# Optimization experiments

Measured on AMD Instinct MI355X. Metric: run time of the kernel, lower is better.

Reference implementation:

```python
import jax, jax.numpy as jnp
import numpy as np

N = 100000; R2 = 500; H = 200; T = 3; E = 300000; R2E = 400000
SE = 4000; SR = 8; S2E = 8000
SLOPE = (1.0 / 8 + 1.0 / 3) / 2  # eval-mode F.rrelu negative slope


def l2norm(x):
    # F.normalize(x) along dim=1 with eps=1e-12
    return x / jnp.maximum(jnp.linalg.norm(x, axis=-1, keepdims=True), 1e-12)


def rrelu(x):
    return jnp.where(x >= 0, x, x * SLOPE)


def seg_mean(vals, seg, num):
    # mean of vals rows grouped by seg id; absent groups stay zero (matches x_input init)
    s = jax.ops.segment_sum(vals, seg, num_segments=num)
    c = jax.ops.segment_sum(jnp.ones((vals.shape[0],), vals.dtype), seg, num_segments=num)
    return s / jnp.maximum(c, 1.0)[:, None]


def lstm_cell(x, h, c, Wih, Whh, bih, bhh):
    g = x @ Wih.T + bih + h @ Whh.T + bhh
    i, f, gg, o = jnp.split(g, 4, axis=1)
    c2 = jax.nn.sigmoid(f) * c + jax.nn.sigmoid(i) * jnp.tanh(gg)
    return jax.nn.sigmoid(o) * jnp.tanh(c2), c2


def gru_cell(x, h, Wih, Whh, bih, bhh):
    gi = x @ Wih.T + bih
    gh = h @ Whh.T + bhh
    ir, iz, inn = jnp.split(gi, 3, axis=1)
    hr, hz, hn = jnp.split(gh, 3, axis=1)
    r = jax.nn.sigmoid(ir + hr)
    z = jax.nn.sigmoid(iz + hz)
    n = jnp.tanh(inn + r * hn)
    return (1 - z) * n + z * h


def rgcn_layer(h, rel_emb, src, dst, et, Wn, Wloop, Wevolve, num_nodes):
    # UnionRGCNLayer: msg = (h_src + rel_emb[etype]) @ W_neighbor, sum-aggregated at dst;
    # self loop uses evolve weight for nodes with in-edges, plain loop weight otherwise.
    msg = (h[src] + rel_emb[et]) @ Wn
    agg = jax.ops.segment_sum(msg, dst, num_segments=num_nodes)
    indeg = jax.ops.segment_sum(jnp.ones((src.shape[0],), h.dtype), dst, num_segments=num_nodes)
    loop = jnp.where((indeg > 0)[:, None], h @ Wevolve, h @ Wloop)
    return rrelu(agg + loop)


def setup_inputs() -> dict:
    key = jax.random.key(0)
    ks = iter(jax.random.split(key, 48))
    s = 1.0 / np.sqrt(H)
    d = {}
    d['src'] = jax.random.randint(next(ks), (T, E), 0, N)
    d['dst'] = jax.random.randint(next(ks), (T, E), 0, N)
    d['etype'] = jax.random.randint(next(ks), (T, E), 0, R2)
    d['r_to_e'] = jax.random.randint(next(ks), (T, R2E), 0, N)
    d['r_seg'] = jax.random.randint(next(ks), (T, R2E), 0, R2)
    d['s_src'] = jax.random.randint(next(ks), (T, SE), 0, R2)
    d['s_dst'] = jax.random.randint(next(ks), (T, SE), 0, R2)
    d['s_etype'] = jax.random.randint(next(ks), (T, SE), 0, SR)
    d['s_r_to_e'] = jax.random.randint(next(ks), (T, S2E), 0, R2)
    d['s_r_seg'] = jax.random.randint(next(ks), (T, S2E), 0, SR)
    d['dynamic_emb'] = jax.random.normal(next(ks), (N, H), jnp.float32)
    d['emb_rel'] = jax.random.normal(next(ks), (R2, H), jnp.float32) * s
    d['p_rel'] = jax.random.normal(next(ks), (SR, H), jnp.float32) * s
    d['Wih1'] = jax.random.normal(next(ks), (4 * H, 2 * H), jnp.float32) * s
    d['Whh1'] = jax.random.normal(next(ks), (4 * H, H), jnp.float32) * s
    d['bih1'] = jax.random.normal(next(ks), (4 * H,), jnp.float32) * s
    d['bhh1'] = jax.random.normal(next(ks), (4 * H,), jnp.float32) * s
    d['Wih2'] = jax.random.normal(next(ks), (4 * H, 2 * H), jnp.float32) * s
    d['Whh2'] = jax.random.normal(next(ks), (4 * H, H), jnp.float32) * s
    d['bih2'] = jax.random.normal(next(ks), (4 * H,), jnp.float32) * s
    d['bhh2'] = jax.random.normal(next(ks), (4 * H,), jnp.float32) * s
    d['Wih3'] = jax.random.normal(next(ks), (3 * H, H), jnp.float32) * s
    d['Whh3'] = jax.random.normal(next(ks), (3 * H, H), jnp.float32) * s
    d['bih3'] = jax.random.normal(next(ks), (3 * H,), jnp.float32) * s
    d['bhh3'] = jax.random.normal(next(ks), (3 * H,), jnp.float32) * s
    d['Wihe'] = jax.random.normal(next(ks), (3 * H, H), jnp.float32) * s
    d['Whhe'] = jax.random.normal(next(ks), (3 * H, H), jnp.float32) * s
    d['bihe'] = jax.random.normal(next(ks), (3 * H,), jnp.float32) * s
    d['bhhe'] = jax.random.normal(next(ks), (3 * H,), jnp.float32) * s
    for nm in ('Wn', 'Wl', 'We', 'sWn', 'sWl', 'sWe'):
        d[nm] = jax.random.normal(next(ks), (2, H, H), jnp.float32) * s
    return d


def reference(src, dst, etype, r_to_e, r_seg, s_src, s_dst, s_etype, s_r_to_e, s_r_seg,
              dynamic_emb, emb_rel, p_rel,
              Wih1, Whh1, bih1, bhh1, Wih2, Whh2, bih2, bhh2,
              Wih3, Whh3, bih3, bhh3, Wihe, Whhe, bihe, bhhe,
              Wn, Wl, We, sWn, sWl, sWe):
    h = l2norm(dynamic_emb)  # layer_norm=True path
    h_0 = c_0 = p_h_0 = p_c_0 = None
    history_embs = []
    rel_embs = []
    for t in range(T):
        # per-relation mean of involved entity embeddings (r_to_e grouped by uniq_r)
        x_input = seg_mean(h[r_to_e[t]], r_seg[t], R2)
        if t == 0:
            h_prev, c_prev = emb_rel, x_input
        else:
            h_prev, c_prev = h_0, c_0
        x_cat = jnp.concatenate([emb_rel, x_input], axis=1)
        h_0, c_0 = lstm_cell(x_cat, h_prev, c_prev, Wih1, Whh1, bih1, bhh1)
        h_0 = l2norm(h_0); c_0 = l2norm(c_0)
        # super-graph: per-super-relation mean of relation embeddings
        sx = seg_mean(h_0[s_r_to_e[t]], s_r_seg[t], SR)
        if t == 0:
            ph_prev, pc_prev = p_rel, sx
        else:
            ph_prev, pc_prev = p_h_0, p_c_0
        sx_cat = jnp.concatenate([p_rel, sx], axis=1)
        p_h_0, p_c_0 = lstm_cell(sx_cat, ph_prev, pc_prev, Wih2, Whh2, bih2, bhh2)
        p_h_0 = l2norm(p_h_0); p_c_0 = l2norm(p_c_0)
        # super RGCN over relation-nodes (2 UnionRGCN layers, same rel emb per layer)
        cur = h_0
        for l in range(2):
            cur = rgcn_layer(cur, p_h_0, s_src[t], s_dst[t], s_etype[t], sWn[l], sWl[l], sWe[l], R2)
        cur = l2norm(cur)
        h_0 = gru_cell(cur, h_0, Wih3, Whh3, bih3, bhh3)
        h_0 = l2norm(h_0)
        rel_embs.append(h_0)
        # entity RGCN over the snapshot graph
        cur_h = h
        for l in range(2):
            cur_h = rgcn_layer(cur_h, h_0, src[t], dst[t], etype[t], Wn[l], Wl[l], We[l], N)
        cur_h = l2norm(cur_h)
        h = gru_cell(cur_h, h, Wihe, Whhe, bihe, bhhe)
        h = l2norm(h)
        history_embs.append(h)
    return jnp.stack(history_embs), jnp.stack(rel_embs)
```

## Files before the change

kernel.cpp:

```cpp
#include <hip/hip_runtime.h>
#include <math.h>

#define N_NODES 100000
#define H 200
#define R2 500
#define T_STEPS 3
#define E_EDGES 300000
#define R2E 400000
#define SE_EDGES 4000
#define SR 8
#define S2E 8000
#define SLOPE 0.22916666666666666f
#define NB 64
#define RCHUNK ((R2E + NB - 1) / NB)
#define NCH 128
#define CHSZ ((N_NODES + NCH - 1) / NCH)
#define SPT  ((CHSZ + 255) / 256)

typedef unsigned short u16;
typedef unsigned int u32;
typedef __bf16 bf8 __attribute__((ext_vector_type(8)));
typedef float f32x4 __attribute__((ext_vector_type(4)));

static __device__ __forceinline__ float fsig(float x) { return 1.f / (1.f + __expf(-x)); }
static __device__ __forceinline__ float ftanh(float x) {
    float e = __expf(-2.f * fabsf(x));
    float t = (1.f - e) / (1.f + e);
    return (x >= 0.f) ? t : -t;
}
static __device__ __forceinline__ float bf2f(u32 lo16) {
    u32 v = lo16 << 16; float f; __builtin_memcpy(&f, &v, 4); return f;
}
static __device__ __forceinline__ u16 f2bf(float a) {
    __bf16 x = (__bf16)a; u16 u; __builtin_memcpy(&u, &x, 2); return u;
}
static __device__ __forceinline__ u32 pk2(float a, float b) {
    return (u32)f2bf(a) | ((u32)f2bf(b) << 16);
}
static __device__ __forceinline__ int xcd_swz(int b, int nwg) {
    int q = nwg >> 3, r = nwg & 7;
    int xcd = b & 7, u = b >> 3;
    int start = xcd * q + (xcd < r ? xcd : r);
    return start + u;
}

__global__ __launch_bounds__(256) void l2norm_k(const float* __restrict__ src, float* __restrict__ dst,
                                                u16* __restrict__ mir, int rows) {
    int wave = threadIdx.x >> 6, lane = threadIdx.x & 63;
    int r = blockIdx.x * 4 + wave;
    if (r >= rows) return;
    float4 v = make_float4(0.f, 0.f, 0.f, 0.f);
    if (lane < 50) v = *(const float4*)(src + (size_t)r * H + lane * 4);
    float s = v.x * v.x + v.y * v.y + v.z * v.z + v.w * v.w;
    for (int o = 32; o > 0; o >>= 1) s += __shfl_down(s, o);
    float rn = 1.f / fmaxf(sqrtf(__shfl(s, 0)), 1e-12f);
    if (lane < 50) {
        float4 o4 = make_float4(v.x * rn, v.y * rn, v.z * rn, v.w * rn);
        *(float4*)(dst + (size_t)r * H + lane * 4) = o4;
        if (mir) {
            uint2 u; u.x = pk2(o4.x, o4.y); u.y = pk2(o4.z, o4.w);
            *(uint2*)(mir + (size_t)r * H + lane * 4) = u;
        }
    }
}

__global__ __launch_bounds__(256) void l2norm_b_k(u16* __restrict__ buf, int rows) {
    int wave = threadIdx.x >> 6, lane = threadIdx.x & 63;
    int r = blockIdx.x * 4 + wave;
    if (r >= rows) return;
    uint2 u = make_uint2(0, 0);
    if (lane < 50) u = *(const uint2*)(buf + (size_t)r * H + lane * 4);
    float x0 = bf2f(u.x & 0xffff), x1 = bf2f(u.x >> 16);
    float x2 = bf2f(u.y & 0xffff), x3 = bf2f(u.y >> 16);
    float s = x0 * x0 + x1 * x1 + x2 * x2 + x3 * x3;
    for (int o = 32; o > 0; o >>= 1) s += __shfl_down(s, o);
    float rn = 1.f / fmaxf(sqrtf(__shfl(s, 0)), 1e-12f);
    if (lane < 50) {
        uint2 o2; o2.x = pk2(x0 * rn, x1 * rn); o2.y = pk2(x2 * rn, x3 * rn);
        *(uint2*)(buf + (size_t)r * H + lane * 4) = o2;
    }
}

__global__ __launch_bounds__(256) void l2norm_bb_k(const u16* __restrict__ src, float* __restrict__ dst,
                                                   u16* __restrict__ mir, int rows) {
    int wave = threadIdx.x >> 6, lane = threadIdx.x & 63;
    int r = blockIdx.x * 4 + wave;
    if (r >= rows) return;
    uint2 u = make_uint2(0, 0);
    if (lane < 50) u = *(const uint2*)(src + (size_t)r * H + lane * 4);
    float x0 = bf2f(u.x & 0xffff), x1 = bf2f(u.x >> 16);
    float x2 = bf2f(u.y & 0xffff), x3 = bf2f(u.y >> 16);
    float s = x0 * x0 + x1 * x1 + x2 * x2 + x3 * x3;
    for (int o = 32; o > 0; o >>= 1) s += __shfl_down(s, o);
    float rn = 1.f / fmaxf(sqrtf(__shfl(s, 0)), 1e-12f);
    if (lane < 50) {
        float4 o4 = make_float4(x0 * rn, x1 * rn, x2 * rn, x3 * rn);
        *(float4*)(dst + (size_t)r * H + lane * 4) = o4;
        uint2 o2; o2.x = pk2(o4.x, o4.y); o2.y = pk2(o4.z, o4.w);
        *(uint2*)(mir + (size_t)r * H + lane * 4) = o2;
    }
}

__global__ void wconv4_k(const float* __restrict__ W0, const float* __restrict__ W1,
                         const float* __restrict__ W2, const float* __restrict__ W3,
                         u16* __restrict__ o) {
    int m = blockIdx.y;
    const float* W = (m == 0) ? W0 : (m == 1) ? W1 : (m == 2) ? W2 : W3;
    int i = blockIdx.x * 256 + threadIdx.x;
    if (i < 40000) { int n = i / 200, k = i - n * 200; o[m * 40000 + i] = f2bf(W[k * 200 + n]); }
}
__global__ void wconv2_k(const float* __restrict__ Wa, const float* __restrict__ Wb, u16* __restrict__ o) {
    int i = blockIdx.x * 256 + threadIdx.x;
    if (i < 240000) o[i] = f2bf(i < 120000 ? Wa[i] : Wb[i - 120000]);
}

__global__ void cnt3_k(const int* __restrict__ d, int total, int per_t, int stride, int* __restrict__ cnt) {
    int i = blockIdx.x * 256 + threadIdx.x;
    if (i < total) { int t = i / per_t; atomicAdd(&cnt[t * stride + d[i]], 1); }
}

__global__ __launch_bounds__(256) void seg_cnt3_k(const int* __restrict__ seg, int per_t, int nseg,
                                                  int blocks_per_t, int* __restrict__ cnt) {
    __shared__ int lc[500];
    int t = blockIdx.x / blocks_per_t;
    int pb = blockIdx.x - t * blocks_per_t;
    const int* s = seg + (size_t)t * per_t;
    int* c = cnt + (size_t)t * nseg;
    for (int i = threadIdx.x; i < nseg; i += 256) lc[i] = 0;
    __syncthreads();
    int chunk = (per_t + blocks_per_t - 1) / blocks_per_t;
    int beg = pb * chunk;
    int end = beg + chunk; if (end > per_t) end = per_t;
    for (int i = beg + threadIdx.x; i < end; i += 256) atomicAdd(&lc[s[i]], 1);
    __syncthreads();
    for (int i = threadIdx.x; i < nseg; i += 256) if (lc[i]) atomicAdd(&c[i], lc[i]);
}

__global__ __launch_bounds__(256) void hist3_k(const int* __restrict__ seg,
                                               int* __restrict__ hist, int* __restrict__ cnt) {
    __shared__ int lc[R2];
    int t = blockIdx.x / NB;
    int pb = blockIdx.x - t * NB;
    const int* s = seg + (size_t)t * R2E;
    for (int i = threadIdx.x; i < R2; i += 256) lc[i] = 0;
    __syncthreads();
    int beg = pb * RCHUNK;
    int end = beg + RCHUNK; if (end > R2E) end = R2E;
    for (int i = beg + threadIdx.x; i < end; i += 256) atomicAdd(&lc[s[i]], 1);
    __syncthreads();
    int* hrow = hist + (size_t)(t * NB + pb) * R2;
    int* c = cnt + (size_t)t * R2;
    for (int i = threadIdx.x; i < R2; i += 256) {
        hrow[i] = lc[i];
        if (lc[i]) atomicAdd(&c[i], lc[i]);
    }
}

__global__ __launch_bounds__(1024) void scan3_k(const int* __restrict__ cntA, int* __restrict__ offA,
                                                int* __restrict__ curA, int n) {
    const int b = blockIdx.x;
    const int* cnt = cntA + (size_t)b * n;
    int* off = offA + (size_t)b * (n + 1);
    int* cur = curA + (size_t)b * n;
    __shared__ int part[1024];
    int tid = threadIdx.x;
    int per = (n + 1023) / 1024;
    int s0 = tid * per;
    int e0 = s0 + per; if (e0 > n) e0 = n;
    int sum = 0;
    for (int i = s0; i < e0; ++i) sum += cnt[i];
    part[tid] = sum;
    __syncthreads();
    for (int d = 1; d < 1024; d <<= 1) {
        int v = (tid >= d) ? part[tid - d] : 0;
        __syncthreads();
        part[tid] += v;
        __syncthreads();
    }
    int excl = (tid == 0) ? 0 : part[tid - 1];
    for (int i = s0; i < e0; ++i) { off[i] = excl; cur[i] = excl; excl += cnt[i]; }
    if (tid == 1023) off[n] = excl;
}

__global__ __launch_bounds__(256) void scanA_k(const int* __restrict__ cntA, int* __restrict__ bsum, int n) {
    int b = blockIdx.x;
    int t = b / NCH, ch = b - t * NCH;
    const int* cnt = cntA + (size_t)t * n;
    int base = ch * CHSZ;
    int cend = base + CHSZ; if (cend > n) cend = n;
    int s0 = base + threadIdx.x * SPT;
    int e0 = s0 + SPT; if (e0 > cend) e0 = cend;
    int sum = 0;
    for (int i = s0; i < e0 && i < cend; ++i) sum += cnt[i];
    __shared__ int red[256];
    red[threadIdx.x] = (s0 < cend) ? sum : 0;
    __syncthreads();
    for (int o = 128; o > 0; o >>= 1) {
        if (threadIdx.x < o) red[threadIdx.x] += red[threadIdx.x + o];
        __syncthreads();
    }
    if (threadIdx.x == 0) bsum[t * NCH + ch] = red[0];
}

__global__ __launch_bounds__(128) void scanB_k(const int* __restrict__ bsum, int* __restrict__ boff,
                                               int* __restrict__ offA, int n) {
    int t = blockIdx.x;
    int tid = threadIdx.x;
    __shared__ int part[128];
    int v = bsum[t * NCH + tid];
    part[tid] = v;
    __syncthreads();
    for (int d = 1; d < 128; d <<= 1) {
        int u = (tid >= d) ? part[tid - d] : 0;
        __syncthreads();
        part[tid] += u;
        __syncthreads();
    }
    boff[t * NCH + tid] = part[tid] - v;
    if (tid == 127) offA[(size_t)t * (n + 1) + n] = part[127];
}

__global__ __launch_bounds__(256) void scanC_k(const int* __restrict__ cntA, const int* __restrict__ boff,
                                               int* __restrict__ offA, int* __restrict__ curA, int n) {
    int b = blockIdx.x;
    int t = b / NCH, ch = b - t * NCH;
    const int* cnt = cntA + (size_t)t * n;
    int* off = offA + (size_t)t * (n + 1);
    int* cur = curA + (size_t)t * n;
    int base = ch * CHSZ;
    int cend = base + CHSZ; if (cend > n) cend = n;
    int s0 = base + threadIdx.x * SPT;
    int e0 = s0 + SPT; if (e0 > cend) e0 = cend;
    int sum = 0;
    for (int i = s0; i < e0 && i < cend; ++i) sum += cnt[i];
    __shared__ int part[256];
    int my = (s0 < cend) ? sum : 0;
    part[threadIdx.x] = my;
    __syncthreads();
    for (int d = 1; d < 256; d <<= 1) {
        int u = (threadIdx.x >= d) ? part[threadIdx.x - d] : 0;
        __syncthreads();
        part[threadIdx.x] += u;
        __syncthreads();
    }
    int excl = boff[t * NCH + ch] + part[threadIdx.x] - my;
    for (int i = s0; i < e0 && i < cend; ++i) {
        off[i] = excl; cur[i] = excl; excl += cnt[i];
    }
}

__global__ __launch_bounds__(64) void offs3_k(const int* __restrict__ hist, const int* __restrict__ csr,
                                              int* __restrict__ offb) {
    int b = blockIdx.x;
    int t = b / R2, s = b - t * R2;
    int lane = threadIdx.x;
    int v = hist[(size_t)(t * NB + lane) * R2 + s];
    int pre = v;
    for (int o = 1; o < 64; o <<= 1) {
        int u = __shfl_up(pre, o);
        if (lane >= o) pre += u;
    }
    int base = csr[(size_t)t * (R2 + 1) + s];
    offb[(size_t)(t * NB + lane) * R2 + s] = base + pre - v;
}

__global__ __launch_bounds__(256) void part3_k(const int* __restrict__ seg, const int* __restrict__ val,
                                               const int* __restrict__ offb, int* __restrict__ outp) {
    __shared__ int cur[R2];
    int t = blockIdx.x / NB;
    int pb = blockIdx.x - t * NB;
    const int* s = seg + (size_t)t * R2E;
    const int* v = val + (size_t)t * R2E;
    const int* ob = offb + (size_t)(t * NB + pb) * R2;
    int* o = outp + (size_t)t * R2E;
    for (int i = threadIdx.x; i < R2; i += 256) cur[i] = ob[i];
    __syncthreads();
    int beg = pb * RCHUNK;
    int end = beg + RCHUNK; if (end > R2E) end = R2E;
    for (int i = beg + threadIdx.x; i < end; i += 256) {
        int p = atomicAdd(&cur[s[i]], 1);
        o[p] = v[i];
    }
}

__global__ void scatter3_k(const int* __restrict__ dst, const int* __restrict__ src,
                           const int* __restrict__ et, int* __restrict__ cur,
                           int* __restrict__ psrc, int* __restrict__ pet,
                           int per_t, int stride, int total) {
    int i = blockIdx.x * 256 + threadIdx.x;
    if (i < total) {
        int t = i / per_t;
        int p = atomicAdd(&cur[t * stride + dst[i]], 1);
        psrc[(size_t)t * per_t + p] = src[i];
        pet[(size_t)t * per_t + p] = et[i];
    }
}

__global__ __launch_bounds__(256) void zlist3b_k(const int* __restrict__ cnt, int* __restrict__ zl,
                                                 int* __restrict__ nz, int n, int bpt) {
    int t = blockIdx.x / bpt;
    int pb = blockIdx.x - t * bpt;
    int i = pb * 256 + threadIdx.x;
    bool z = (i < n) && (cnt[(size_t)t * n + i] == 0);
    unsigned long long mask = __ballot(z);
    int wave = threadIdx.x >> 6, lane = threadIdx.x & 63;
    __shared__ int wbase[4];
    __shared__ int bbase;
    if (lane == 0) wbase[wave] = __popcll(mask);
    __syncthreads();
    if (threadIdx.x == 0) {
        int s0 = wbase[0], s1 = wbase[1], s2 = wbase[2], s3 = wbase[3];
        int tot = s0 + s1 + s2 + s3;
        bbase = tot ? atomicAdd(&nz[t], tot) : 0;
        wbase[0] = 0; wbase[1] = s0; wbase[2] = s0 + s1; wbase[3] = s0 + s1 + s2;
    }
    __syncthreads();
    if (z) {
        int off = bbase + wbase[wave] + __popcll(mask & ((1ull << lane) - 1ull));
        zl[(size_t)t * n + off] = i;
    }
}

#define SEG_CW 25
__global__ __launch_bounds__(256) void seg_acc_k(const float* __restrict__ hsrc,
                                                 const int* __restrict__ idx,
                                                 const int* __restrict__ seg, int n,
                                                 float* __restrict__ acc, int nseg) {
    __shared__ float lacc[500 * SEG_CW];
    int cg = blockIdx.x & 7;
    int pb = blockIdx.x >> 3;
    int NPB = gridDim.x >> 3;
    int t = threadIdx.x;
    for (int i = t; i < nseg * SEG_CW; i += 256) lacc[i] = 0.f;
    __syncthreads();
    int chunk = (n + NPB - 1) / NPB;
    int beg = pb * chunk;
    int end = beg + chunk; if (end > n) end = n;
    if (t < 250) {
        int il = t / SEG_CW;
        int c = t - il * SEG_CW;
        int col = cg * SEG_CW + c;
        for (int i = beg + il; i < end; i += 10) {
            int r = seg[i];
            int e = idx[i];
            atomicAdd(&lacc[r * SEG_CW + c], hsrc[(size_t)e * H + col]);
        }
    }
    __syncthreads();
    for (int i = t; i < nseg * SEG_CW; i += 256) {
        int r = i / SEG_CW, c = i - (i / SEG_CW) * SEG_CW;
        atomicAdd(&acc[(size_t)r * H + cg * SEG_CW + c], lacc[i]);
    }
}

__global__ void seg_div_k(float* __restrict__ acc, const int* __restrict__ cnt, int rows) {
    int i = blockIdx.x * blockDim.x + threadIdx.x;
    if (i < rows * H) {
        int c = cnt[i / H];
        acc[i] /= (float)(c > 0 ? c : 1);
    }
}

__global__ __launch_bounds__(256) void seg_mean_part_k(const u16* __restrict__ h,
                                                       const int* __restrict__ per,
                                                       const int* __restrict__ off,
                                                       float* __restrict__ xacc, int nseg) {
    int r = blockIdx.x >> 2;
    int p = blockIdx.x & 3;
    if (r >= nseg) return;
    int wv = threadIdx.x >> 6, lane = threadIdx.x & 63;
    int beg = off[r], end = off[r + 1];
    float a0 = 0.f, a1 = 0.f, a2 = 0.f, a3 = 0.f;
    for (int i = beg + p * 4 + wv; i < end; i += 16) {
        int e = per[i];
        if (lane < 50) {
            uint2 u = ((const uint2*)(h + (size_t)e * H))[lane];
            a0 += bf2f(u.x & 0xffff); a1 += bf2f(u.x >> 16);
            a2 += bf2f(u.y & 0xffff); a3 += bf2f(u.y >> 16);
        }
    }
    __shared__ float red[4][200];
    if (lane < 50) *(float4*)(&red[wv][lane * 4]) = make_float4(a0, a1, a2, a3);
    __syncthreads();
    int t = threadIdx.x;
    if (t < 200) {
        float s = red[0][t] + red[1][t] + red[2][t] + red[3][t];
        atomicAdd(&xacc[(size_t)r * H + t], s);
    }
}
__global__ void seg_fin_k(float* __restrict__ acc, const int* __restrict__ off, int nseg) {
    int i = blockIdx.x * 256 + threadIdx.x;
    if (i < nseg * H) {
        int r = i / H;
        int c = off[r + 1] - off[r];
        acc[i] /= (float)(c > 0 ? c : 1);
    }
}

__global__ __launch_bounds__(256) void lstm_k(const float* __restrict__ x1, const float* __restrict__ x2,
                                              const float* __restrict__ hprev, const float* __restrict__ cprev,
                                              const float* __restrict__ Wih, const float* __restrict__ Whh,
                                              const float* __restrict__ bih, const float* __restrict__ bhh,
                                              float* __restrict__ hout, float* __restrict__ cout, int rows) {
    int r = blockIdx.x;
    if (r >= rows) return;
    __shared__ float xb[2 * H], hb[H], gb[4 * H], hv[H], cv[H];
    __shared__ float red[8];
    int t = threadIdx.x;
    for (int i = t; i < 2 * H; i += 256)
        xb[i] = (i < H) ? x1[(size_t)r * H + i] : x2[(size_t)r * H + i - H];
    if (t < H) hb[t] = hprev[(size_t)r * H + t];
    __syncthreads();
    for (int j = t; j < 4 * H; j += 256) {
        float s = bih[j] + bhh[j];
        const float* wi = Wih + (size_t)j * 2 * H;
        for (int k = 0; k < 2 * H; ++k) s += xb[k] * wi[k];
        const float* wh = Whh + (size_t)j * H;
        for (int k = 0; k < H; ++k) s += hb[k] * wh[k];
        gb[j] = s;
    }
    __syncthreads();
    if (t < H) {
        float ig = fsig(gb[t]);
        float fg = fsig(gb[H + t]);
        float gg = ftanh(gb[2 * H + t]);
        float og = fsig(gb[3 * H + t]);
        float c2 = fg * cprev[(size_t)r * H + t] + ig * gg;
        cv[t] = c2;
        hv[t] = og * ftanh(c2);
    }
    __syncthreads();
    float sh = 0.f, sc = 0.f;
    if (t < H) { sh = hv[t] * hv[t]; sc = cv[t] * cv[t]; }
    for (int o = 32; o > 0; o >>= 1) { sh += __shfl_down(sh, o); sc += __shfl_down(sc, o); }
    if ((t & 63) == 0) { red[t >> 6] = sh; red[4 + (t >> 6)] = sc; }
    __syncthreads();
    if (t == 0) {
        red[0] = 1.f / fmaxf(sqrtf(red[0] + red[1] + red[2] + red[3]), 1e-12f);
        red[4] = 1.f / fmaxf(sqrtf(red[4] + red[5] + red[6] + red[7]), 1e-12f);
    }
    __syncthreads();
    if (t < H) {
        hout[(size_t)r * H + t] = hv[t] * red[0];
        cout[(size_t)r * H + t] = cv[t] * red[4];
    }
}

__global__ __launch_bounds__(256) void gru_small_k(const float* __restrict__ x, const float* __restrict__ h,
                                                   const float* __restrict__ Wih, const float* __restrict__ Whh,
                                                   const float* __restrict__ bih, const float* __restrict__ bhh,
                                                   float* __restrict__ outp, u16* __restrict__ mirp, int rows) {
    int r = blockIdx.x;
    if (r >= rows) return;
    __shared__ float xb[H], hb[H], gi[3 * H], gh[3 * H], ov[H];
    __shared__ float red[4];
    int t = threadIdx.x;
    if (t < H) { xb[t] = x[(size_t)r * H + t]; hb[t] = h[(size_t)r * H + t]; }
    __syncthreads();
    for (int j = t; j < 3 * H; j += 256) {
        float si = bih[j], sh2 = bhh[j];
        const float* wi = Wih + (size_t)j * H;
        const float* wh = Whh + (size_t)j * H;
        for (int k = 0; k < H; ++k) { si += xb[k] * wi[k]; sh2 += hb[k] * wh[k]; }
        gi[j] = si; gh[j] = sh2;
    }
    __syncthreads();
    if (t < H) {
        float rr = fsig(gi[t] + gh[t]);
        float zz = fsig(gi[H + t] + gh[H + t]);
        float nn = ftanh(gi[2 * H + t] + rr * gh[2 * H + t]);
        ov[t] = (1.f - zz) * nn + zz * hb[t];
    }
    __syncthreads();
    float s = (t < H) ? ov[t] * ov[t] : 0.f;
    for (int o = 32; o > 0; o >>= 1) s += __shfl_down(s, o);
    if ((t & 63) == 0) red[t >> 6] = s;
    __syncthreads();
    if (t == 0) red[0] = 1.f / fmaxf(sqrtf(red[0] + red[1] + red[2] + red[3]), 1e-12f);
    __syncthreads();
    if (t < H) {
        float v = ov[t] * red[0];
        outp[(size_t)r * H + t] = v;
        mirp[(size_t)r * H + t] = f2bf(v);
    }
}

__global__ __launch_bounds__(256) void sup_agg_csr_k(const float* __restrict__ cur, const float* __restrict__ prel,
                                                     const int* __restrict__ soff, const int* __restrict__ sssrc,
                                                     const int* __restrict__ sset, float* __restrict__ sagg) {
    int r = blockIdx.x;
    int t = threadIdx.x;
    if (t >= H) return;
    int beg = soff[r], end = soff[r + 1];
    float acc = 0.f;
    for (int i = beg; i < end; ++i) {
        int s = sssrc[i], et = sset[i];
        acc += cur[(size_t)s * H + t] + prel[(size_t)et * H + t];
    }
    sagg[(size_t)r * H + t] = acc;
}

__global__ __launch_bounds__(256) void sup_comb_k(const float* __restrict__ agg, const float* __restrict__ cur,
                                                  const float* __restrict__ Wn, const float* __restrict__ We,
                                                  const float* __restrict__ Wl, const int* __restrict__ indeg,
                                                  float* __restrict__ outp) {
    int r = blockIdx.x;
    __shared__ float ar[H], cr[H];
    int t = threadIdx.x;
    if (t < H) { ar[t] = agg[(size_t)r * H + t]; cr[t] = cur[(size_t)r * H + t]; }
    __syncthreads();
    const float* W2 = (indeg[r] > 0) ? We : Wl;
    if (t < H) {
        float s = 0.f;
        for (int k = 0; k < H; ++k) s += ar[k] * Wn[(size_t)k * H + t] + cr[k] * W2[(size_t)k * H + t];
        outp[(size_t)r * H + t] = (s >= 0.f) ? s : s * SLOPE;
    }
}

__global__ __launch_bounds__(256) void ent_agg_b_k(const u16* __restrict__ cur, const u16* __restrict__ rel,
                                                   const int* __restrict__ eoff, const int* __restrict__ esrc,
                                                   const int* __restrict__ eet, u16* __restrict__ agg, int n) {
    int wave = threadIdx.x >> 6, lane = threadIdx.x & 63;
    int v = blockIdx.x * 4 + wave;
    if (v >= n) return;
    float a0 = 0.f, a1 = 0.f, a2 = 0.f, a3 = 0.f;
    bool act = lane < 50;
    int beg = eoff[v], end = eoff[v + 1];
    int i = beg;
    for (; i + 2 <= end; i += 2) {
        int e0 = esrc[i], t0 = eet[i];
        int e1 = esrc[i + 1], t1 = eet[i + 1];
        if (act) {
            uint2 h0 = ((const uint2*)(cur + (size_t)e0 * H))[lane];
            uint2 h1 = ((const uint2*)(cur + (size_t)e1 * H))[lane];
            uint2 r0 = ((const uint2*)(rel + (size_t)t0 * H))[lane];
            uint2 r1 = ((const uint2*)(rel + (size_t)t1 * H))[lane];
            a0 += bf2f(h0.x & 0xffff) + bf2f(r0.x & 0xffff) + bf2f(h1.x & 0xffff) + bf2f(r1.x & 0xffff);
            a1 += bf2f(h0.x >> 16) + bf2f(r0.x >> 16) + bf2f(h1.x >> 16) + bf2f(r1.x >> 16);
            a2 += bf2f(h0.y & 0xffff) + bf2f(r0.y & 0xffff) + bf2f(h1.y & 0xffff) + bf2f(r1.y & 0xffff);
            a3 += bf2f(h0.y >> 16) + bf2f(r0.y >> 16) + bf2f(h1.y >> 16) + bf2f(r1.y >> 16);
        }
    }
    if (i < end) {
        int e0 = esrc[i], t0 = eet[i];
        if (act) {
            uint2 h0 = ((const uint2*)(cur + (size_t)e0 * H))[lane];
            uint2 r0 = ((const uint2*)(rel + (size_t)t0 * H))[lane];
            a0 += bf2f(h0.x & 0xffff) + bf2f(r0.x & 0xffff);
            a1 += bf2f(h0.x >> 16) + bf2f(r0.x >> 16);
            a2 += bf2f(h0.y & 0xffff) + bf2f(r0.y & 0xffff);
            a3 += bf2f(h0.y >> 16) + bf2f(r0.y >> 16);
        }
    }
    if (act) {
        uint2 o; o.x = pk2(a0, a1); o.y = pk2(a2, a3);
        ((uint2*)(agg + (size_t)v * H))[lane] = o;
    }
}

#define BSTR 108
__global__ __launch_bounds__(128) void gemm_bp_k(const u16* __restrict__ A1, const u16* __restrict__ A2,
                                                 const u16* __restrict__ B1, const u16* __restrict__ B2,
                                                 u16* __restrict__ Cm, int M, int Nc) {
    __shared__ __bf16 Bs[64 * BSTR];
    const int tid = threadIdx.x;
    int idx2 = xcd_swz(blockIdx.x, gridDim.x);
    const int m0 = (idx2 >> 2) * 128;
    const int n0 = (idx2 & 3) * 64;
    const int w = tid >> 6, lane = tid & 63;
    const int lr = lane & 15, lo = lane >> 4;
    const int mbase = m0 + w * 64;

    bf8 zb;
#pragma unroll
    for (int e = 0; e < 8; ++e) zb[e] = (__bf16)0.f;

    f32x4 acc[4][4];
#pragma unroll
    for (int i = 0; i < 4; ++i)
#pragma unroll
        for (int j = 0; j < 4; ++j)
#pragma unroll
            for (int e = 0; e < 4; ++e) acc[i][j][e] = 0.f;

    auto stageB = [&](const u16* Bp, int kbase, int nch) {
        for (int ch = tid; ch < 64 * nch; ch += 128) {
            int n = ch / nch, q = ch - n * nch;
            int ng = n0 + n;
            uint4 v = make_uint4(0, 0, 0, 0);
            if (ng < Nc) v = *(const uint4*)(Bp + (size_t)ng * 200 + kbase + q * 8);
            *(uint4*)(&Bs[n * BSTR + q * 8]) = v;
        }
    };
    auto loadA = [&](bf8* buf, const u16* Ap, int kt7) {
        int kk = kt7 * 32 + lo * 8;
        bool kv = kk < 200;
#pragma unroll
        for (int mf = 0; mf < 4; ++mf) {
            int m = mbase + mf * 16 + lr;
            bf8 v = zb;
            if (kv && m < M) v = *(const bf8*)(Ap + (size_t)m * 200 + kk);
            buf[mf] = v;
        }
    };
    auto mmaStep = [&](bf8* a, int kt7, int kbase) {
        int kk = kt7 * 32 + lo * 8;
        int kcl = (kk < 200) ? (kk - kbase) : 0;
#pragma unroll
        for (int nf = 0; nf < 4; ++nf) {
            bf8 b = *(const bf8*)(&Bs[(nf * 16 + lr) * BSTR + kcl]);
#pragma unroll
            for (int mf = 0; mf < 4; ++mf)
                acc[mf][nf] = __builtin_amdgcn_mfma_f32_16x16x32_bf16(a[mf], b, acc[mf][nf], 0, 0, 0);
        }
    };

    bf8 a0[4], a1[4];
    stageB(B1, 0, 12);
    __syncthreads();
    loadA(a0, A1, 0);
    loadA(a1, A1, 1); mmaStep(a0, 0, 0);
    loadA(a0, A1, 2); mmaStep(a1, 1, 0);
    loadA(a1, A1, 3); mmaStep(a0, 2, 0);
    __syncthreads();
    stageB(B1, 96, 13);
    __syncthreads();
    loadA(a0, A1, 4); mmaStep(a1, 3, 96);
    loadA(a1, A1, 5); mmaStep(a0, 4, 96);
    loadA(a0, A1, 6); mmaStep(a1, 5, 96);
    loadA(a1, A2, 0); mmaStep(a0, 6, 96);
    __syncthreads();
    stageB(B2, 0, 12);
    __syncthreads();
    loadA(a0, A2, 1); mmaStep(a1, 0, 0);
    loadA(a1, A2, 2); mmaStep(a0, 1, 0);
    loadA(a0, A2, 3); mmaStep(a1, 2, 0);
    __syncthreads();
    stageB(B2, 96, 13);
    __syncthreads();
    loadA(a1, A2, 4); mmaStep(a0, 3, 96);
    loadA(a0, A2, 5); mmaStep(a1, 4, 96);
    loadA(a1, A2, 6); mmaStep(a0, 5, 96);
    mmaStep(a1, 6, 96);

#pragma unroll
    for (int mf = 0; mf < 4; ++mf) {
#pragma unroll
        for (int r = 0; r < 4; ++r) {
            int m = mbase + mf * 16 + lo * 4 + r;
            if (m >= M) continue;
#pragma unroll
            for (int nf = 0; nf < 4; ++nf) {
                int n = n0 + nf * 16 + lr;
                if (n >= Nc) continue;
                float v = acc[mf][nf][r];
                v = (v >= 0.f) ? v : v * SLOPE;
                Cm[(size_t)m * Nc + n] = f2bf(v);
            }
        }
    }
}

__global__ __launch_bounds__(256) void fixup_b_k(const u16* __restrict__ h, const float* __restrict__ Wl,
                                                 const int* __restrict__ zl, const int* __restrict__ nz,
                                                 u16* __restrict__ outp) {
    __shared__ float xr[H];
    int nzv = *nz;
    for (int z = blockIdx.x; z < nzv; z += gridDim.x) {
        int row = zl[z];
        if (threadIdx.x < H) xr[threadIdx.x] = bf2f(h[(size_t)row * H + threadIdx.x]);
        __syncthreads();
        if (threadIdx.x < H) {
            float s = 0.f;
            for (int k = 0; k < H; ++k) s += xr[k] * Wl[(size_t)k * H + threadIdx.x];
            outp[(size_t)row * H + threadIdx.x] = f2bf((s >= 0.f) ? s : s * SLOPE);
        }
        __syncthreads();
    }
}

#define GCG2 13
#define GTPB 3
#define WSTR 204
__global__ __launch_bounds__(256, 4) void gru_wlds_k(const u16* __restrict__ Xb, const u16* __restrict__ Hb,
                                                     const u16* __restrict__ Wb,
                                                     const float* __restrict__ bih, const float* __restrict__ bhh,
                                                     u16* __restrict__ Outb, int M) {
    __shared__ __bf16 Ws[6][16 * WSTR];
    const int tid = threadIdx.x;
    int idx2 = xcd_swz(blockIdx.x, gridDim.x);
    const int cg = idx2 % GCG2;
    const int rb = idx2 / GCG2;
    const int w = tid >> 6, lane = tid & 63;
    const int lr = lane & 15, lo = lane >> 4;
    const int c0 = cg * 16;

    for (int ch = tid; ch < 2400; ch += 256) {
        int s = ch / 400;
        int rem = ch - s * 400;
        int col = rem / 25, q = rem - (rem / 25) * 25;
        int cc = c0 + col; if (cc > 199) cc = 199;
        uint4 v = *(const uint4*)(Wb + (size_t)(s * 200 + cc) * 200 + q * 8);
        *(uint4*)(&Ws[s][col * WSTR + q * 8]) = v;
    }
    __syncthreads();

    int c = c0 + lr;
    const bool cvalid = c < 200;
    const int cc = cvalid ? c : 199;
    const float b0 = bih[cc], b1 = bih[200 + cc], b2 = bih[400 + cc];
    const float b3 = bhh[cc], b4 = bhh[200 + cc], b5 = bhh[400 + cc];

    bf8 zb;
#pragma unroll
    for (int e = 0; e < 8; ++e) zb[e] = (__bf16)0.f;

    for (int tile = 0; tile < GTPB; ++tile) {
        int mbase = (rb * GTPB + tile) * 128 + w * 32;
        if (mbase >= M) break;
        int m0r = mbase + lr;      if (m0r >= M) m0r = M - 1;
        int m1r = mbase + 16 + lr; if (m1r >= M) m1r = M - 1;
        const u16* Xp0 = Xb + (size_t)m0r * 200 + lo * 8;
        const u16* Xp1 = Xb + (size_t)m1r * 200 + lo * 8;
        const u16* Hp0 = Hb + (size_t)m0r * 200 + lo * 8;
        const u16* Hp1 = Hb + (size_t)m1r * 200 + lo * 8;

        f32x4 acc[6][2];
#pragma unroll
        for (int s = 0; s < 6; ++s)
#pragma unroll
            for (int i = 0; i < 2; ++i)
#pragma unroll
                for (int e = 0; e < 4; ++e) acc[s][i][e] = 0.f;

#pragma unroll
        for (int kt = 0; kt < 7; ++kt) {
            const int koff = kt * 32;
            const bool kv = (kt < 6) || (lo == 0);
            const int kcl = kv ? (koff + lo * 8) : 0;
            bf8 xa0 = zb, xa1 = zb, ha0 = zb, ha1 = zb;
            if (kv) {
                xa0 = *(const bf8*)(Xp0 + koff);
                xa1 = *(const bf8*)(Xp1 + koff);
                ha0 = *(const bf8*)(Hp0 + koff);
                ha1 = *(const bf8*)(Hp1 + koff);
            }
#pragma unroll
            for (int s = 0; s < 6; ++s) {
                bf8 wv = *(const bf8*)(&Ws[s][lr * WSTR + kcl]);
                bf8 a0f = (s < 3) ? xa0 : ha0;
                bf8 a1f = (s < 3) ? xa1 : ha1;
                acc[s][0] = __builtin_amdgcn_mfma_f32_16x16x32_bf16(a0f, wv, acc[s][0], 0, 0, 0);
                acc[s][1] = __builtin_amdgcn_mfma_f32_16x16x32_bf16(a1f, wv, acc[s][1], 0, 0, 0);
            }
        }
        if (cvalid) {
#pragma unroll
            for (int mf = 0; mf < 2; ++mf) {
#pragma unroll
                for (int r = 0; r < 4; ++r) {
                    int m = mbase + mf * 16 + lo * 4 + r;
                    if (m >= M) continue;
                    float ir = acc[0][mf][r] + b0;
                    float iz = acc[1][mf][r] + b1;
                    float in_ = acc[2][mf][r] + b2;
                    float hr = acc[3][mf][r] + b3;
                    float hz = acc[4][mf][r] + b4;
                    float hn = acc[5][mf][r] + b5;
                    float rr = fsig(ir + hr);
                    float zz = fsig(iz + hz);
                    float nn = ftanh(in_ + rr * hn);
                    float hvv = bf2f(Hb[(size_t)m * 200 + c]);
                    Outb[(size_t)m * 200 + c] = f2bf((1.f - zz) * nn + zz * hvv);
                }
            }
        }
    }
}

extern "C" void kernel_launch(void* const* d_in, const int* in_sizes, int n_in,
                              void* d_out, int out_size, void* d_ws, size_t ws_size,
                              hipStream_t stream) {
    (void)in_sizes; (void)n_in; (void)out_size; (void)ws_size;
    const int* src  = (const int*)d_in[0];
    const int* dst  = (const int*)d_in[1];
    const int* etyp = (const int*)d_in[2];
    const int* rte  = (const int*)d_in[3];
    const int* rseg = (const int*)d_in[4];
    const int* ssrc = (const int*)d_in[5];
    const int* sdst = (const int*)d_in[6];
    const int* setp = (const int*)d_in[7];
    const int* srte = (const int*)d_in[8];
    const int* srseg= (const int*)d_in[9];
    const float* dyn     = (const float*)d_in[10];
    const float* emb_rel = (const float*)d_in[11];
    const float* p_rel   = (const float*)d_in[12];
    const float* Wih1 = (const float*)d_in[13]; const float* Whh1 = (const float*)d_in[14];
    const float* bih1 = (const float*)d_in[15]; const float* bhh1 = (const float*)d_in[16];
    const float* Wih2 = (const float*)d_in[17]; const float* Whh2 = (const float*)d_in[18];
    const float* bih2 = (const float*)d_in[19]; const float* bhh2 = (const float*)d_in[20];
    const float* Wih3 = (const float*)d_in[21]; const float* Whh3 = (const float*)d_in[22];
    const float* bih3 = (const float*)d_in[23]; const float* bhh3 = (const float*)d_in[24];
    const float* Wihe = (const float*)d_in[25]; const float* Whhe = (const float*)d_in[26];
    const float* bihe = (const float*)d_in[27]; const float* bhhe = (const float*)d_in[28];
    const float* Wn  = (const float*)d_in[29];
    const float* Wl  = (const float*)d_in[30];
    const float* We  = (const float*)d_in[31];
    const float* sWn = (const float*)d_in[32];
    const float* sWl = (const float*)d_in[33];
    const float* sWe = (const float*)d_in[34];

    float* out = (float*)d_out;
    const size_t NH = (size_t)N_NODES * H;
    float* relout = out + 3 * NH;

    char* wp = (char*)d_ws;
    auto carve = [&](size_t bytes) -> void* {
        void* p = (void*)wp;
        wp += (bytes + 255) & ~(size_t)255;
        return p;
    };
    u16* aggB = (u16*)carve(NH * 2);
    u16* m0b  = (u16*)carve(NH * 2);
    u16* m1b  = (u16*)carve(NH * 2);
    u16* hmir = (u16*)carve(NH * 2);
    u16* gob  = (u16*)carve(NH * 2);
    u16* relm = (u16*)carve((size_t)R2 * H * 2);
    u16* wtB  = (u16*)carve((size_t)400000 * 2);
    float* h0a  = (float*)carve((size_t)R2 * H * 4);
    float* c0b  = (float*)carve((size_t)R2 * H * 4);
    float* xin  = (float*)carve((size_t)R2 * H * 4);
    float* srelA= (float*)carve((size_t)R2 * H * 4);
    float* srelB= (float*)carve((size_t)R2 * H * 4);
    float* sagg = (float*)carve((size_t)R2 * H * 4);
    float* sxin = (float*)carve((size_t)SR * H * 4);
    float* p_h  = (float*)carve((size_t)SR * H * 4);
    float* p_c  = (float*)carve((size_t)SR * H * 4);
    int* eoff3  = (int*)carve((size_t)3 * (N_NODES + 1) * 4);
    int* esrcp3 = (int*)carve((size_t)3 * E_EDGES * 4);
    int* eetp3  = (int*)carve((size_t)3 * E_EDGES * 4);
    int* zl3    = (int*)carve((size_t)3 * N_NODES * 4);
    int* nz3    = (int*)carve(3 * 4);
    int* rcsr3  = (int*)carve((size_t)3 * (R2 + 1) * 4);
    int* rper3  = (int*)carve((size_t)3 * R2E * 4);
    int* sindeg3= (int*)carve((size_t)3 * R2 * 4);
    int* scnt3  = (int*)carve((size_t)3 * SR * 4);
    int* hist3  = (int*)carve((size_t)3 * NB * R2 * 4);
    int* offb3  = (int*)carve((size_t)3 * NB * R2 * 4);
    int* soff3  = (int*)carve((size_t)3 * (R2 + 1) * 4);
    int* scur3  = (int*)carve((size_t)3 * R2 * 4);
    int* sssrc3 = (int*)carve((size_t)3 * SE_EDGES * 4);
    int* sset3  = (int*)carve((size_t)3 * SE_EDGES * 4);
    int* bsum3  = (int*)carve((size_t)3 * NCH * 4);
    int* boff3  = (int*)carve((size_t)3 * NCH * 4);
    int* ecnt3 = (int*)m0b;
    int* rcnt3 = (int*)m0b + 3 * N_NODES;
    int* ecur3 = (int*)aggB;
    int* rcur3 = (int*)aggB + 3 * N_NODES;

    dim3 wg4(157, 4);
    wconv4_k<<<wg4, 256, 0, stream>>>(Wn, We, Wn + 40000, We + 40000, wtB);
    wconv2_k<<<938, 256, 0, stream>>>(Wihe, Whhe, wtB + 160000);

    hipMemsetAsync(ecnt3, 0, (size_t)3 * N_NODES * 4, stream);
    hipMemsetAsync(rcnt3, 0, (size_t)3 * R2 * 4, stream);
    hipMemsetAsync(nz3, 0, 3 * 4, stream);
    hipMemsetAsync(sindeg3, 0, (size_t)3 * R2 * 4, stream);
    hipMemsetAsync(scnt3, 0, (size_t)3 * SR * 4, stream);
    cnt3_k<<<(3 * E_EDGES + 255) / 256, 256, 0, stream>>>(dst, 3 * E_EDGES, E_EDGES, N_NODES, ecnt3);
    scanA_k<<<3 * NCH, 256, 0, stream>>>(ecnt3, bsum3, N_NODES);
    scanB_k<<<3, 128, 0, stream>>>(bsum3, boff3, eoff3, N_NODES);
    scanC_k<<<3 * NCH, 256, 0, stream>>>(ecnt3, boff3, eoff3, ecur3, N_NODES);
    scatter3_k<<<(3 * E_EDGES + 255) / 256, 256, 0, stream>>>(dst, src, etyp, ecur3, esrcp3, eetp3,
                                                             E_EDGES, N_NODES, 3 * E_EDGES);
    {
        int bpt = (N_NODES + 255) / 256;
        zlist3b_k<<<3 * bpt, 256, 0, stream>>>(ecnt3, zl3, nz3, N_NODES, bpt);
    }
    hist3_k<<<3 * NB, 256, 0, stream>>>(rseg, hist3, rcnt3);
    scan3_k<<<3, 1024, 0, stream>>>(rcnt3, rcsr3, rcur3, R2);
    offs3_k<<<3 * R2, 64, 0, stream>>>(hist3, rcsr3, offb3);
    part3_k<<<3 * NB, 256, 0, stream>>>(rseg, rte, offb3, rper3);
    seg_cnt3_k<<<12, 256, 0, stream>>>(srseg, S2E, SR, 4, scnt3);
    cnt3_k<<<(3 * SE_EDGES + 255) / 256, 256, 0, stream>>>(sdst, 3 * SE_EDGES, SE_EDGES, R2, sindeg3);
    scan3_k<<<3, 1024, 0, stream>>>(sindeg3, soff3, scur3, R2);
    scatter3_k<<<(3 * SE_EDGES + 255) / 256, 256, 0, stream>>>(sdst, ssrc, setp, scur3, sssrc3, sset3,
                                                              SE_EDGES, R2, 3 * SE_EDGES);

    l2norm_k<<<(N_NODES + 3) / 4, 256, 0, stream>>>(dyn, out + NH, hmir, N_NODES);

    const int gw  = 4 * ((N_NODES + 127) / 128);
    const int NRB2 = (N_NODES + GTPB * 128 - 1) / (GTPB * 128);
    const int gwg = GCG2 * NRB2;

    for (int t = 0; t < T_STEPS; ++t) {
        const int* srte_t = srte + (size_t)t * S2E;
        const int* srseg_t= srseg + (size_t)t * S2E;
        const int* eoff_t = eoff3 + (size_t)t * (N_NODES + 1);
        const int* esrc_t = esrcp3 + (size_t)t * E_EDGES;
        const int* eet_t  = eetp3 + (size_t)t * E_EDGES;
        const int* zl_t   = zl3 + (size_t)t * N_NODES;
        const int* nz_t   = nz3 + t;
        const int* rcsr_t = rcsr3 + (size_t)t * (R2 + 1);
        const int* rper_t = rper3 + (size_t)t * R2E;
        const int* sind_t = sindeg3 + (size_t)t * R2;
        const int* scnt_t = scnt3 + (size_t)t * SR;
        const int* soff_t = soff3 + (size_t)t * (R2 + 1);
        const int* sssrc_t= sssrc3 + (size_t)t * SE_EDGES;
        const int* sset_t = sset3 + (size_t)t * SE_EDGES;

        float* hist = out + (size_t)t * NH;
        float* rel_t = relout + (size_t)t * R2 * H;
        const float* hprev = (t == 0) ? emb_rel : relout + (size_t)(t - 1) * R2 * H;
        const float* cprev = (t == 0) ? xin : c0b;
        const float* php   = (t == 0) ? p_rel : p_h;
        const float* pcp   = (t == 0) ? sxin : p_c;

        hipMemsetAsync(xin, 0, (size_t)R2 * H * 4, stream);
        seg_mean_part_k<<<R2 * 4, 256, 0, stream>>>(hmir, rper_t, rcsr_t, xin, R2);
        seg_fin_k<<<(R2 * H + 255) / 256, 256, 0, stream>>>(xin, rcsr_t, R2);
        lstm_k<<<R2, 256, 0, stream>>>(emb_rel, xin, hprev, cprev, Wih1, Whh1, bih1, bhh1, h0a, c0b, R2);
        hipMemsetAsync(sxin, 0, (size_t)SR * H * 4, stream);
        seg_acc_k<<<16 * 8, 256, 0, stream>>>(h0a, srte_t, srseg_t, S2E, sxin, SR);
        seg_div_k<<<(SR * H + 255) / 256, 256, 0, stream>>>(sxin, scnt_t, SR);
        lstm_k<<<SR, 256, 0, stream>>>(p_rel, sxin, php, pcp, Wih2, Whh2, bih2, bhh2, p_h, p_c, SR);
        sup_agg_csr_k<<<R2, 256, 0, stream>>>(h0a, p_h, soff_t, sssrc_t, sset_t, sagg);
        sup_comb_k<<<R2, 256, 0, stream>>>(sagg, h0a, sWn, sWe, sWl, sind_t, srelA);
        sup_agg_csr_k<<<R2, 256, 0, stream>>>(srelA, p_h, soff_t, sssrc_t, sset_t, sagg);
        sup_comb_k<<<R2, 256, 0, stream>>>(sagg, srelA, sWn + H * H, sWe + H * H, sWl + H * H, sind_t, srelB);
        l2norm_k<<<(R2 + 3) / 4, 256, 0, stream>>>(srelB, srelB, (u16*)nullptr, R2);
        gru_small_k<<<R2, 256, 0, stream>>>(srelB, h0a, Wih3, Whh3, bih3, bhh3, rel_t, relm, R2);

        ent_agg_b_k<<<(N_NODES + 3) / 4, 256, 0, stream>>>(hmir, relm, eoff_t, esrc_t, eet_t, aggB, N_NODES);
        gemm_bp_k<<<gw, 128, 0, stream>>>(aggB, hmir, wtB, wtB + 40000, m0b, N_NODES, H);
        fixup_b_k<<<2048, 256, 0, stream>>>(hmir, Wl, zl_t, nz_t, m0b);
        ent_agg_b_k<<<(N_NODES + 3) / 4, 256, 0, stream>>>(m0b, relm, eoff_t, esrc_t, eet_t, aggB, N_NODES);
        gemm_bp_k<<<gw, 128, 0, stream>>>(aggB, m0b, wtB + 80000, wtB + 120000, m1b, N_NODES, H);
        fixup_b_k<<<2048, 256, 0, stream>>>(m0b, Wl + H * H, zl_t, nz_t, m1b);
        l2norm_b_k<<<(N_NODES + 3) / 4, 256, 0, stream>>>(m1b, N_NODES);

        gru_wlds_k<<<gwg, 256, 0, stream>>>(m1b, hmir, wtB + 160000, bihe, bhhe, gob, N_NODES);
        l2norm_bb_k<<<(N_NODES + 3) / 4, 256, 0, stream>>>(gob, hist, hmir, N_NODES);
    }
}
```

Measured before the change: 2.666 ms.

## Fuse super-graph aggregate and combine, drop atomics in seg-mean, retune GRU tiles

The super-RGCN CSR aggregation is merged into the combine kernel, which removes two launches per step and the intermediate aggregate buffer round trip. The relation segment-mean now writes four per-partition partial sums that the finalize kernel adds, replacing the memset and atomicAdd accumulation. The GRU kernel's tiles-per-block constant is doubled. These are small-kernel launch and atomic savings plus a tiling change, and the new GRU tile count could affect occupancy or tail balance.

```diff
diff --git a/kernel.cpp b/kernel.cpp
--- a/kernel.cpp
+++ b/kernel.cpp
@@ -364,7 +364,7 @@
 __global__ __launch_bounds__(256) void seg_mean_part_k(const u16* __restrict__ h,
                                                        const int* __restrict__ per,
                                                        const int* __restrict__ off,
-                                                       float* __restrict__ xacc, int nseg) {
+                                                       float* __restrict__ xpart, int nseg) {
     int r = blockIdx.x >> 2;
     int p = blockIdx.x & 3;
     if (r >= nseg) return;
@@ -385,15 +385,18 @@
     int t = threadIdx.x;
     if (t < 200) {
         float s = red[0][t] + red[1][t] + red[2][t] + red[3][t];
-        atomicAdd(&xacc[(size_t)r * H + t], s);
-    }
-}
-__global__ void seg_fin_k(float* __restrict__ acc, const int* __restrict__ off, int nseg) {
+        xpart[((size_t)p * nseg + r) * H + t] = s;
+    }
+}
+__global__ void seg_fin_k(const float* __restrict__ xpart, const int* __restrict__ off,
+                          float* __restrict__ acc, int nseg) {
     int i = blockIdx.x * 256 + threadIdx.x;
     if (i < nseg * H) {
         int r = i / H;
+        size_t stride = (size_t)nseg * H;
+        float s = xpart[i] + xpart[stride + i] + xpart[2 * stride + i] + xpart[3 * stride + i];
         int c = off[r + 1] - off[r];
-        acc[i] /= (float)(c > 0 ? c : 1);
+        acc[i] = s / (float)(c > 0 ? c : 1);
     }
 }
 
@@ -485,29 +488,23 @@
     }
 }
 
-__global__ __launch_bounds__(256) void sup_agg_csr_k(const float* __restrict__ cur, const float* __restrict__ prel,
-                                                     const int* __restrict__ soff, const int* __restrict__ sssrc,
-                                                     const int* __restrict__ sset, float* __restrict__ sagg) {
-    int r = blockIdx.x;
-    int t = threadIdx.x;
-    if (t >= H) return;
-    int beg = soff[r], end = soff[r + 1];
-    float acc = 0.f;
-    for (int i = beg; i < end; ++i) {
-        int s = sssrc[i], et = sset[i];
-        acc += cur[(size_t)s * H + t] + prel[(size_t)et * H + t];
-    }
-    sagg[(size_t)r * H + t] = acc;
-}
-
-__global__ __launch_bounds__(256) void sup_comb_k(const float* __restrict__ agg, const float* __restrict__ cur,
-                                                  const float* __restrict__ Wn, const float* __restrict__ We,
-                                                  const float* __restrict__ Wl, const int* __restrict__ indeg,
-                                                  float* __restrict__ outp) {
+__global__ __launch_bounds__(256) void sup_fused_k(const float* __restrict__ cur, const float* __restrict__ prel,
+                                                   const int* __restrict__ soff, const int* __restrict__ sssrc,
+                                                   const int* __restrict__ sset,
+                                                   const float* __restrict__ Wn, const float* __restrict__ We,
+                                                   const float* __restrict__ Wl, const int* __restrict__ indeg,
+                                                   float* __restrict__ outp) {
     int r = blockIdx.x;
     __shared__ float ar[H], cr[H];
     int t = threadIdx.x;
-    if (t < H) { ar[t] = agg[(size_t)r * H + t]; cr[t] = cur[(size_t)r * H + t]; }
+    if (t < H) {
+        int beg = soff[r], end = soff[r + 1];
+        float acc = 0.f;
+        for (int i = beg; i < end; ++i)
+            acc += cur[(size_t)sssrc[i] * H + t] + prel[(size_t)sset[i] * H + t];
+        ar[t] = acc;
+        cr[t] = cur[(size_t)r * H + t];
+    }
     __syncthreads();
     const float* W2 = (indeg[r] > 0) ? We : Wl;
     if (t < H) {
@@ -680,7 +677,7 @@
 }
 
 #define GCG2 13
-#define GTPB 3
+#define GTPB 6
 #define WSTR 204
 __global__ __launch_bounds__(256, 4) void gru_wlds_k(const u16* __restrict__ Xb, const u16* __restrict__ Hb,
                                                      const u16* __restrict__ Wb,
@@ -830,9 +827,9 @@
     float* h0a  = (float*)carve((size_t)R2 * H * 4);
     float* c0b  = (float*)carve((size_t)R2 * H * 4);
     float* xin  = (float*)carve((size_t)R2 * H * 4);
+    float* xpart= (float*)carve((size_t)4 * R2 * H * 4);
     float* srelA= (float*)carve((size_t)R2 * H * 4);
     float* srelB= (float*)carve((size_t)R2 * H * 4);
-    float* sagg = (float*)carve((size_t)R2 * H * 4);
     float* sxin = (float*)carve((size_t)SR * H * 4);
     float* p_h  = (float*)carve((size_t)SR * H * 4);
     float* p_c  = (float*)carve((size_t)SR * H * 4);
@@ -916,18 +913,16 @@
         const float* php   = (t == 0) ? p_rel : p_h;
         const float* pcp   = (t == 0) ? sxin : p_c;
 
-        hipMemsetAsync(xin, 0, (size_t)R2 * H * 4, stream);
-        seg_mean_part_k<<<R2 * 4, 256, 0, stream>>>(hmir, rper_t, rcsr_t, xin, R2);
-        seg_fin_k<<<(R2 * H + 255) / 256, 256, 0, stream>>>(xin, rcsr_t, R2);
+        seg_mean_part_k<<<R2 * 4, 256, 0, stream>>>(hmir, rper_t, rcsr_t, xpart, R2);
+        seg_fin_k<<<(R2 * H + 255) / 256, 256, 0, stream>>>(xpart, rcsr_t, xin, R2);
         lstm_k<<<R2, 256, 0, stream>>>(emb_rel, xin, hprev, cprev, Wih1, Whh1, bih1, bhh1, h0a, c0b, R2);
         hipMemsetAsync(sxin, 0, (size_t)SR * H * 4, stream);
         seg_acc_k<<<16 * 8, 256, 0, stream>>>(h0a, srte_t, srseg_t, S2E, sxin, SR);
         seg_div_k<<<(SR * H + 255) / 256, 256, 0, stream>>>(sxin, scnt_t, SR);
         lstm_k<<<SR, 256, 0, stream>>>(p_rel, sxin, php, pcp, Wih2, Whh2, bih2, bhh2, p_h, p_c, SR);
-        sup_agg_csr_k<<<R2, 256, 0, stream>>>(h0a, p_h, soff_t, sssrc_t, sset_t, sagg);
-        sup_comb_k<<<R2, 256, 0, stream>>>(sagg, h0a, sWn, sWe, sWl, sind_t, srelA);
-        sup_agg_csr_k<<<R2, 256, 0, stream>>>(srelA, p_h, soff_t, sssrc_t, sset_t, sagg);
-        sup_comb_k<<<R2, 256, 0, stream>>>(sagg, srelA, sWn + H * H, sWe + H * H, sWl + H * H, sind_t, srelB);
+        sup_fused_k<<<R2, 256, 0, stream>>>(h0a, p_h, soff_t, sssrc_t, sset_t, sWn, sWe, sWl, sind_t, srelA);
+        sup_fused_k<<<R2, 256, 0, stream>>>(srelA, p_h, soff_t, sssrc_t, sset_t,
+                                            sWn + H * H, sWe + H * H, sWl + H * H, sind_t, srelB);
         l2norm_k<<<(R2 + 3) / 4, 256, 0, stream>>>(srelB, srelB, (u16*)nullptr, R2);
         gru_small_k<<<R2, 256, 0, stream>>>(srelB, h0a, Wih3, Whh3, bih3, bhh3, rel_t, relm, R2);
 
```

Result: no change. 2.641 ms (-0.9%).
